# Kernel optimization log

Hardware: AMD Instinct MI355X
Metric: run time of the kernel (lower is better)

Reference implementation:

```python
import jax, jax.numpy as jnp
import numpy as np

D_MODEL = 1024
N_HIDDEN = 64   # per-head dim (outer factor of packed proj dim)
N_HEAD = 16
B, L = 2, 2048


def setup_inputs() -> dict:
    key = jax.random.key(0)
    ks = jax.random.split(key, 7)
    s = 0.02
    return {
        "q": jax.random.normal(ks[0], (B, L, D_MODEL), dtype=jnp.float32),
        "k": jax.random.normal(ks[1], (B, L, D_MODEL), dtype=jnp.float32),
        "v": jax.random.normal(ks[2], (B, L, D_MODEL), dtype=jnp.float32),
        # torch nn.Linear weights: shape (out_features, in_features), y = x @ W.T
        "W_Q": jax.random.normal(ks[3], (N_HIDDEN * N_HEAD, D_MODEL), dtype=jnp.float32) * s,
        "W_K": jax.random.normal(ks[4], (N_HIDDEN * N_HEAD, D_MODEL), dtype=jnp.float32) * s,
        "W_V": jax.random.normal(ks[5], (N_HIDDEN * N_HEAD, D_MODEL), dtype=jnp.float32) * s,
        "W_O": jax.random.normal(ks[6], (D_MODEL, N_HEAD * N_HIDDEN), dtype=jnp.float32) * s,
    }


def reference(q, k, v, W_Q, W_K, W_V, W_O):
    b, l, _ = q.shape
    # projections (bias=False)
    qp = q @ W_Q.T  # [b,l,n_hidden*n_head]
    kp = k @ W_K.T
    vp = v @ W_V.T
    # rearrange 'b l (c h) -> b l c h' with c=n_hidden: hidden is OUTER factor
    qh = qp.reshape(b, l, N_HIDDEN, N_HEAD)
    kh = kp.reshape(b, l, N_HIDDEN, N_HEAD)
    vh = vp.reshape(b, l, N_HIDDEN, N_HEAD)
    scores = jnp.einsum('bldh,bjdh->bhlj', qh, kh) / np.float32(np.sqrt(N_HIDDEN))
    attn = jax.nn.softmax(scores, axis=-1)
    out = jnp.einsum('bhlj,bjdh->bldh', attn, vh)  # [b,l,n_hidden,n_head]
    out = out.reshape(b, l, N_HIDDEN * N_HEAD)      # 'b l d h -> b l (d h)'
    return out @ W_O.T
```

## Files before the change

### kernel.cpp

```cpp
#include <hip/hip_runtime.h>
#include <hip/hip_bf16.h>
#include <stdint.h>

typedef __attribute__((ext_vector_type(8))) short short8;
typedef __attribute__((ext_vector_type(4))) float f32x4;
typedef __attribute__((ext_vector_type(16))) float f32x16;
typedef __attribute__((ext_vector_type(2))) int int2v;
typedef unsigned short u16;
typedef unsigned int u32;


#define WAIT_VM12() do { asm volatile("s_waitcnt vmcnt(12)" ::: "memory"); \
                         __builtin_amdgcn_sched_barrier(0); } while (0)
#define WAIT_VM8()  do { asm volatile("s_waitcnt vmcnt(8)" ::: "memory"); \
                         __builtin_amdgcn_sched_barrier(0); } while (0)
#define WAIT_VM0()  do { asm volatile("s_waitcnt vmcnt(0)" ::: "memory"); \
                         __builtin_amdgcn_sched_barrier(0); } while (0)
#define BARRIER()   do { __builtin_amdgcn_s_barrier(); \
                         __builtin_amdgcn_sched_barrier(0); } while (0)
#define LGKM0_BAR() do { asm volatile("s_waitcnt lgkmcnt(0)" ::: "memory"); \
                         __builtin_amdgcn_s_barrier(); \
                         __builtin_amdgcn_sched_barrier(0); } while (0)

__device__ __forceinline__ u16 bf16rne(float f) {
  u32 u = __builtin_bit_cast(u32, f);
  u += 0x7FFFu + ((u >> 16) & 1u);
  return (u16)(u >> 16);
}

__device__ __forceinline__ u32 cvtpk(float lo, float hi) {
  u32 r;
  asm("v_cvt_pk_bf16_f32 %0, %1, %2" : "=v"(r) : "v"(lo), "v"(hi));
  return r;
}

__device__ __forceinline__ void gl_lds16(const u16* g, u16* l) {
  __builtin_amdgcn_global_load_lds((const __attribute__((address_space(1))) void*)g,
                                   (__attribute__((address_space(3))) void*)l, 16, 0, 0);
}

struct CastArgs {
  const float* src[4];
  u16* dst[4];
  int n4[4];
};

__global__ void cast_all(CastArgs a) {
  const int id = blockIdx.y;
  const float* __restrict__ s = a.src[id];
  u16* __restrict__ d = a.dst[id];
  const int stride = gridDim.x * blockDim.x;
  const int i0 = blockIdx.x * blockDim.x + threadIdx.x;
  if (id < 3) {
    const int n4 = a.n4[id];
    for (int i = i0; i < n4; i += stride) {
      float4 v = ((const float4*)s)[i];
      u32 lo = (u32)bf16rne(v.x) | ((u32)bf16rne(v.y) << 16);
      u32 hi = (u32)bf16rne(v.z) | ((u32)bf16rne(v.w) << 16);
      ((uint2*)d)[i] = make_uint2(lo, hi);
    }
  } else {
    const int n = a.n4[3];
    for (int i = i0; i < n; i += stride) {
      int row = i >> 10, c = i & 1023;
      int hh = c >> 6, dd = c & 63;
      d[i] = bf16rne(s[(row << 10) + dd * 16 + hh]);
    }
  }
}

struct ProjFArgs { const float* A[3]; const u16* W[3]; u16* D[3]; float scale[3]; };

__global__ __launch_bounds__(256, 2) void gemm_projf(ProjFArgs pa) {
  const int bid = blockIdx.x;
  const int grp = ((bid >> 6) << 3) | (bid & 7);
  const int bn = ((bid >> 3) & 7) * 128;
  const int z = grp >> 5;
  const int bm = (grp & 31) * 128;
  const float* __restrict__ A = pa.A[z];
  const u16* __restrict__ Bw = pa.W[z];
  u16* __restrict__ D = pa.D[z];
  const float ascale = pa.scale[z];
  const int epi = (z == 2) ? 1 : 0;

  const int tid = threadIdx.x, lane = tid & 63, w = tid >> 6;
  const int wr = w >> 1, wc = w & 1;
  __shared__ __align__(16) u16 As[2][128 * 64];
  __shared__ __align__(16) u16 Bs[2][128 * 64];

  f32x4 acc[4][4];
#pragma unroll
  for (int m = 0; m < 4; ++m)
#pragma unroll
    for (int n = 0; n < 4; ++n) acc[m][n] = (f32x4){0.f, 0.f, 0.f, 0.f};

  struct ARegs { float4 v[8]; };
  ARegs RA, RB;

  auto STAGE_A = [&](int kt, ARegs& R) {
#pragma unroll
    for (int i = 0; i < 4; ++i) {
      int c = tid + i * 256;
      int row = c >> 3;
      int col = (((c & 7) ^ (row & 7)) << 3);
      const float* src = A + (size_t)(bm + row) * 1024 + kt * 64 + col;
      R.v[2 * i] = *(const float4*)(src);
      R.v[2 * i + 1] = *(const float4*)(src + 4);
    }
  };
  auto WRITE_A = [&](ARegs& R, int b) {
#pragma unroll
    for (int i = 0; i < 4; ++i) {
      int c = tid + i * 256;
      u32 p0 = (u32)bf16rne(R.v[2 * i].x) | ((u32)bf16rne(R.v[2 * i].y) << 16);
      u32 p1 = (u32)bf16rne(R.v[2 * i].z) | ((u32)bf16rne(R.v[2 * i].w) << 16);
      u32 p2 = (u32)bf16rne(R.v[2 * i + 1].x) | ((u32)bf16rne(R.v[2 * i + 1].y) << 16);
      u32 p3 = (u32)bf16rne(R.v[2 * i + 1].z) | ((u32)bf16rne(R.v[2 * i + 1].w) << 16);
      *(uint4*)&As[b][c * 8] = make_uint4(p0, p1, p2, p3);
    }
  };
  auto STAGE_B = [&](int kt, int b) {
#pragma unroll
    for (int i = 0; i < 4; ++i) {
      int c = tid + i * 256;
      int row = c >> 3;
      int swz = (((c & 7) ^ (row & 7)) << 3);
      gl_lds16(Bw + (size_t)(bn + row) * 1024 + kt * 64 + swz, &Bs[b][c * 8]);
    }
  };
  auto COMPUTE = [&](int b) {
#pragma unroll
    for (int ks = 0; ks < 2; ++ks) {
      const int ck = ks * 4 + (lane >> 4);
      short8 af[4], bfr[4];
#pragma unroll
      for (int m = 0; m < 4; ++m) {
        int r = wr * 64 + m * 16 + (lane & 15);
        af[m] = *(const short8*)&As[b][(r * 8 + (ck ^ (r & 7))) * 8];
      }
#pragma unroll
      for (int n = 0; n < 4; ++n) {
        int r = wc * 64 + n * 16 + (lane & 15);
        bfr[n] = *(const short8*)&Bs[b][(r * 8 + (ck ^ (r & 7))) * 8];
      }
#pragma unroll
      for (int m = 0; m < 4; ++m)
#pragma unroll
        for (int n = 0; n < 4; ++n)
          acc[m][n] = __builtin_amdgcn_mfma_f32_16x16x32_bf16(af[m], bfr[n], acc[m][n], 0, 0, 0);
    }
  };

  STAGE_A(0, RA); STAGE_B(0, 0);
  STAGE_A(1, RB); STAGE_B(1, 1);
  for (int k2 = 0; k2 < 7; ++k2) {
    const int kt = 2 * k2;
    WAIT_VM12();
    WRITE_A(RA, 0); LGKM0_BAR();
    COMPUTE(0); BARRIER();
    STAGE_A(kt + 2, RA); STAGE_B(kt + 2, 0);
    WAIT_VM12();
    WRITE_A(RB, 1); LGKM0_BAR();
    COMPUTE(1); BARRIER();
    STAGE_A(kt + 3, RB); STAGE_B(kt + 3, 1);
  }
  WAIT_VM12();
  WRITE_A(RA, 0); LGKM0_BAR();
  COMPUTE(0); BARRIER();
  WAIT_VM0();
  WRITE_A(RB, 1); LGKM0_BAR();
  COMPUTE(1);

  const int lrow4 = (lane >> 4) << 2;
  const int h = lane & 15;
  if (epi == 0) {
    const int dbase = (bn + wc * 64) >> 4;
#pragma unroll
    for (int m = 0; m < 4; ++m)
#pragma unroll
      for (int i = 0; i < 4; ++i) {
        int R = bm + wr * 64 + m * 16 + lrow4 + i;
        int b = R >> 11, l = R & 2047;
        u32 lo = (u32)bf16rne(acc[m][0][i] * ascale) | ((u32)bf16rne(acc[m][1][i] * ascale) << 16);
        u32 hi = (u32)bf16rne(acc[m][2][i] * ascale) | ((u32)bf16rne(acc[m][3][i] * ascale) << 16);
        size_t addr = ((size_t)((b * 16 + h) * 2048 + l)) * 64 + dbase;
        *(uint2*)(D + addr) = make_uint2(lo, hi);
      }
  } else {
    const int dbase = (bn + wc * 64) >> 4;
    const int b = bm >> 11;
#pragma unroll
    for (int m = 0; m < 4; ++m) {
      int l0 = (bm & 2047) + wr * 64 + m * 16 + lrow4;
#pragma unroll
      for (int n = 0; n < 4; ++n) {
        int d = dbase + n;
        u32 lo = (u32)bf16rne(acc[m][n][0]) | ((u32)bf16rne(acc[m][n][1]) << 16);
        u32 hi = (u32)bf16rne(acc[m][n][2]) | ((u32)bf16rne(acc[m][n][3]) << 16);
        size_t addr = ((size_t)((b * 16 + h) * 64 + d)) * 2048 + l0;
        *(uint2*)(D + addr) = make_uint2(lo, hi);
      }
    }
  }
}

__global__ __launch_bounds__(256, 2) void gemm_oproj(const u16* __restrict__ A,
                                                     const u16* __restrict__ Bw,
                                                     float* __restrict__ C) {
  const int bn = blockIdx.x * 128, bm = blockIdx.y * 128;
  const int tid = threadIdx.x, lane = tid & 63, w = tid >> 6;
  const int wr = w >> 1, wc = w & 1;
  __shared__ __align__(16) u16 As[2][128 * 64];
  __shared__ __align__(16) u16 Bs[2][128 * 64];
  f32x4 acc[4][4];
#pragma unroll
  for (int m = 0; m < 4; ++m)
#pragma unroll
    for (int n = 0; n < 4; ++n) acc[m][n] = (f32x4){0.f, 0.f, 0.f, 0.f};

  auto STAGE = [&](int kt, int b) {
#pragma unroll
    for (int i = 0; i < 4; ++i) {
      int c = tid + i * 256;
      int row = c >> 3, kc = c & 7;
      int swz = (kc ^ (row & 7)) << 3;
      int bA = bm >> 11;
      int lrow = (bm & 2047) + row;
      const u16* srcA = A + ((size_t)(bA * 16 + kt) * 2048 + lrow) * 64 + swz;
      gl_lds16(srcA, &As[b][c * 8]);
      const u16* srcB = Bw + (size_t)(bn + row) * 1024 + kt * 64 + swz;
      gl_lds16(srcB, &Bs[b][c * 8]);
    }
  };

  auto COMPUTE = [&](int b) {
#pragma unroll
    for (int ks = 0; ks < 2; ++ks) {
      const int ck = ks * 4 + (lane >> 4);
      short8 af[4], bfr[4];
#pragma unroll
      for (int m = 0; m < 4; ++m) {
        int r = wr * 64 + m * 16 + (lane & 15);
        af[m] = *(const short8*)&As[b][(r * 8 + (ck ^ (r & 7))) * 8];
      }
#pragma unroll
      for (int n = 0; n < 4; ++n) {
        int r = wc * 64 + n * 16 + (lane & 15);
        bfr[n] = *(const short8*)&Bs[b][(r * 8 + (ck ^ (r & 7))) * 8];
      }
#pragma unroll
      for (int m = 0; m < 4; ++m)
#pragma unroll
        for (int n = 0; n < 4; ++n)
          acc[m][n] = __builtin_amdgcn_mfma_f32_16x16x32_bf16(af[m], bfr[n], acc[m][n], 0, 0, 0);
    }
  };

  STAGE(0, 0);
  STAGE(1, 1);
  for (int kt = 0; kt < 15; ++kt) {
    WAIT_VM8();
    BARRIER();
    COMPUTE(kt & 1);
    BARRIER();
    if (kt < 14) STAGE(kt + 2, kt & 1);
  }
  WAIT_VM0();
  BARRIER();
  COMPUTE(1);

  const int lrow4 = (lane >> 4) << 2;
#pragma unroll
  for (int m = 0; m < 4; ++m)
#pragma unroll
    for (int i = 0; i < 4; ++i) {
      int R = bm + wr * 64 + m * 16 + lrow4 + i;
      size_t base = (size_t)R * 1024 + bn + wc * 64 + (lane & 15);
#pragma unroll
      for (int n = 0; n < 4; ++n) C[base + n * 16] = acc[m][n][i];
    }
}

__global__ __launch_bounds__(128, 2) void attn_kernel(const u16* __restrict__ Qh,
                                                      const u16* __restrict__ Kh,
                                                      const u16* __restrict__ Vt,
                                                      u16* __restrict__ Oh) {
  const int hb = blockIdx.x;
  const int qt = blockIdx.y;
  const int tid = threadIdx.x, lane = tid & 63, w = tid >> 6;
  const int l31 = lane & 31, hi = lane >> 5;
  __shared__ __align__(16) u16 Ks[2][64 * 64];
  __shared__ __align__(16) u16 Vs[3][64 * 64];

  const u16* Qg = Qh + (size_t)hb * (2048 * 64);
  const u16* Kg = Kh + (size_t)hb * (2048 * 64);
  const u16* Vg = Vt + (size_t)hb * (64 * 2048);
  const int qrow = qt * 64 + w * 32 + l31;

  short8 qf[4];
#pragma unroll
  for (int ks = 0; ks < 4; ++ks)
    qf[ks] = *(const short8*)(Qg + (size_t)qrow * 64 + ks * 16 + hi * 8);

  int rs[4], sw[4];
#pragma unroll
  for (int i = 0; i < 4; ++i) {
    int c = tid + i * 128;
    rs[i] = c >> 3;
    sw[i] = (((c & 7) ^ (rs[i] & 7)) << 3);
  }

  auto STAGE_K = [&](int t, int slot) {
    const size_t ko = (size_t)t * (64 * 64);
#pragma unroll
    for (int i = 0; i < 4; ++i) {
      int c = tid + i * 128;
      gl_lds16(Kg + ko + (size_t)rs[i] * 64 + sw[i], &Ks[slot][c * 8]);
    }
  };
  auto STAGE_V = [&](int t, int slot) {
    const int vo = t * 64;
#pragma unroll
    for (int i = 0; i < 4; ++i) {
      int c = tid + i * 128;
      gl_lds16(Vg + (size_t)rs[i] * 2048 + vo + sw[i], &Vs[slot][c * 8]);
    }
  };

  f32x16 oacc0, oacc1, SA0, SA1, SB0, SB1;
#pragma unroll
  for (int i = 0; i < 16; ++i) { oacc0[i] = 0.f; oacc1[i] = 0.f; }
  u32 pkA[16], pkB[16];
  float lrow = 0.f;

  auto QKT = [&](int kslot, f32x16& s0, f32x16& s1) {
#pragma unroll
    for (int i = 0; i < 16; ++i) { s0[i] = 0.f; s1[i] = 0.f; }
    __builtin_amdgcn_s_setprio(1);
#pragma unroll
    for (int ks = 0; ks < 4; ++ks) {
      const int ck = 2 * ks + hi;
      const int r0 = l31, r1 = 32 + l31;
      short8 k0 = *(const short8*)&Ks[kslot][(r0 * 8 + (ck ^ (r0 & 7))) * 8];
      short8 k1 = *(const short8*)&Ks[kslot][(r1 * 8 + (ck ^ (r1 & 7))) * 8];
      s0 = __builtin_amdgcn_mfma_f32_32x32x16_bf16(k0, qf[ks], s0, 0, 0, 0);
      s1 = __builtin_amdgcn_mfma_f32_32x32x16_bf16(k1, qf[ks], s1, 0, 0, 0);
    }
    __builtin_amdgcn_s_setprio(0);
  };

  auto PV = [&](const u32* pk, int vslot) {
    __builtin_amdgcn_s_setprio(1);
#pragma unroll
    for (int c = 0; c < 4; ++c) {
      union { u32 wu[4]; short8 v; } un;
      un.wu[0] = pk[c * 4 + 0]; un.wu[1] = pk[c * 4 + 1];
      un.wu[2] = pk[c * 4 + 2]; un.wu[3] = pk[c * 4 + 3];
      const int ckv = 2 * c + hi;
      const int rv0 = l31, rv1 = 32 + l31;
      short8 v0 = *(const short8*)&Vs[vslot][(rv0 * 8 + (ckv ^ (rv0 & 7))) * 8];
      short8 v1 = *(const short8*)&Vs[vslot][(rv1 * 8 + (ckv ^ (rv1 & 7))) * 8];
      oacc0 = __builtin_amdgcn_mfma_f32_32x32x16_bf16(v0, un.v, oacc0, 0, 0, 0);
      oacc1 = __builtin_amdgcn_mfma_f32_32x32x16_bf16(v1, un.v, oacc1, 0, 0, 0);
    }
    __builtin_amdgcn_s_setprio(0);
  };

  auto SOFTMAX = [&](f32x16& s0, f32x16& s1, u32* pk) {
#pragma unroll
    for (int i = 0; i < 16; ++i) {
      s0[i] = __builtin_amdgcn_exp2f(s0[i]);
      s1[i] = __builtin_amdgcn_exp2f(s1[i]);
    }
    f32x16 a01 = s0 + s1;
    float r8[8];
#pragma unroll
    for (int i = 0; i < 8; ++i) r8[i] = a01[i] + a01[i + 8];
#pragma unroll
    for (int i = 0; i < 4; ++i) r8[i] += r8[i + 4];
    float rsum = (r8[0] + r8[1]) + (r8[2] + r8[3]);
    int2v pr = __builtin_amdgcn_permlane32_swap(__builtin_bit_cast(int, rsum),
                                                __builtin_bit_cast(int, rsum), false, false);
    lrow += __builtin_bit_cast(float, pr[0]) + __builtin_bit_cast(float, pr[1]);
#pragma unroll
    for (int c = 0; c < 4; ++c) {
      float pe0, pe1, pe2, pe3, pe4, pe5, pe6, pe7;
      if (c < 2) {
        const int s8 = (c & 1) * 8;
        pe0 = s0[s8 + 0]; pe1 = s0[s8 + 1]; pe2 = s0[s8 + 2]; pe3 = s0[s8 + 3];
        pe4 = s0[s8 + 4]; pe5 = s0[s8 + 5]; pe6 = s0[s8 + 6]; pe7 = s0[s8 + 7];
      } else {
        const int s8 = (c & 1) * 8;
        pe0 = s1[s8 + 0]; pe1 = s1[s8 + 1]; pe2 = s1[s8 + 2]; pe3 = s1[s8 + 3];
        pe4 = s1[s8 + 4]; pe5 = s1[s8 + 5]; pe6 = s1[s8 + 6]; pe7 = s1[s8 + 7];
      }
      u32 a0 = cvtpk(pe0, pe1), a1 = cvtpk(pe2, pe3);
      u32 a2 = cvtpk(pe4, pe5), a3 = cvtpk(pe6, pe7);
      int2v w02 = __builtin_amdgcn_permlane32_swap((int)a0, (int)a2, false, false);
      int2v w13 = __builtin_amdgcn_permlane32_swap((int)a1, (int)a3, false, false);
      pk[c * 4 + 0] = (u32)w02[0]; pk[c * 4 + 1] = (u32)w13[0];
      pk[c * 4 + 2] = (u32)w02[1]; pk[c * 4 + 3] = (u32)w13[1];
    }
  };

  STAGE_K(0, 0); STAGE_K(1, 1); STAGE_V(0, 0);
  WAIT_VM8(); BARRIER();
  QKT(0, SA0, SA1);
  BARRIER();
  STAGE_K(2, 0); STAGE_V(1, 1);
  WAIT_VM8(); BARRIER();
  QKT(1, SB0, SB1);
  SOFTMAX(SA0, SA1, pkB);
  BARRIER();
  STAGE_K(3, 1); STAGE_V(2, 2);

  for (int i = 2; i < 32; i += 2) {
    WAIT_VM8(); BARRIER();
    QKT(0, SA0, SA1);
    PV(pkB, (i - 2) % 3);
    SOFTMAX(SB0, SB1, pkA);
    BARRIER();
    if (i + 2 <= 31) STAGE_K(i + 2, 0);
    STAGE_V(i + 1, (i + 1) % 3);
    WAIT_VM8(); BARRIER();
    QKT(1, SB0, SB1);
    PV(pkA, (i - 1) % 3);
    SOFTMAX(SA0, SA1, pkB);
    BARRIER();
    if (i + 3 <= 31) STAGE_K(i + 3, 1);
    if (i + 2 <= 31) STAGE_V(i + 2, (i + 2) % 3);
  }

  WAIT_VM0(); BARRIER();
  SOFTMAX(SB0, SB1, pkA);
  PV(pkB, 30 % 3);
  PV(pkA, 31 % 3);

  const float inv = 1.0f / lrow;
  u16* Og = Oh + (size_t)hb * (2048 * 64) + (size_t)qrow * 64;
#pragma unroll
  for (int dblk = 0; dblk < 2; ++dblk) {
#pragma unroll
    for (int r = 0; r < 16; r += 2) {
      const int d = dblk * 32 + (r & 3) + 8 * (r >> 2) + 4 * hi;
      float v0 = (dblk ? oacc1[r] : oacc0[r]) * inv;
      float v1 = (dblk ? oacc1[r + 1] : oacc0[r + 1]) * inv;
      *(u32*)(Og + d) = (u32)bf16rne(v0) | ((u32)bf16rne(v1) << 16);
    }
  }
}

extern "C" void kernel_launch(void* const* d_in, const int* in_sizes, int n_in,
                              void* d_out, int out_size, void* d_ws, size_t ws_size,
                              hipStream_t stream) {
  const float* q = (const float*)d_in[0];
  const float* k = (const float*)d_in[1];
  const float* v = (const float*)d_in[2];
  const float* WQ = (const float*)d_in[3];
  const float* WK = (const float*)d_in[4];
  const float* WV = (const float*)d_in[5];
  const float* WO = (const float*)d_in[6];
  float* out = (float*)d_out;
  char* ws = (char*)d_ws;
  const size_t MB = 1024 * 1024;
  if (ws_size < 64 * MB) return;

  u16* WQb = (u16*)(ws + 24 * MB);
  u16* WKb = (u16*)(ws + 26 * MB);
  u16* WVb = (u16*)(ws + 28 * MB);
  u16* WOt = (u16*)(ws + 30 * MB);
  u16* Qh  = (u16*)(ws + 32 * MB);
  u16* Kh  = (u16*)(ws + 40 * MB);
  u16* Vt  = (u16*)(ws + 48 * MB);
  u16* Ohd = (u16*)(ws + 56 * MB);

  CastArgs ca;
  ca.src[0] = WQ; ca.dst[0] = WQb; ca.n4[0] = (1024 * 1024) / 4;
  ca.src[1] = WK; ca.dst[1] = WKb; ca.n4[1] = (1024 * 1024) / 4;
  ca.src[2] = WV; ca.dst[2] = WVb; ca.n4[2] = (1024 * 1024) / 4;
  ca.src[3] = WO; ca.dst[3] = WOt; ca.n4[3] = 1024 * 1024;
  cast_all<<<dim3(128, 4), 256, 0, stream>>>(ca);

  ProjFArgs pa;
  pa.A[0] = q; pa.W[0] = WQb; pa.D[0] = Qh;  pa.scale[0] = 0.18033688011f;
  pa.A[1] = k; pa.W[1] = WKb; pa.D[1] = Kh;  pa.scale[1] = 1.0f;
  pa.A[2] = v; pa.W[2] = WVb; pa.D[2] = Vt;  pa.scale[2] = 1.0f;
  gemm_projf<<<768, 256, 0, stream>>>(pa);

  attn_kernel<<<dim3(32, 32), 128, 0, stream>>>(Qh, Kh, Vt, Ohd);

  gemm_oproj<<<dim3(8, 32), 256, 0, stream>>>(Ohd, WOt, out);
}
```

Before: 131.1 us.

## Split attention KV range across two blocks and merge with atomics

The attention kernel now uses 256-thread blocks covering 128 query rows and splits the key/value sequence into two halves along a new grid dimension. Each block accumulates unnormalized outputs and row sums into fp32 workspace via atomicAdd. A new normalization kernel then divides by the summed row sum and packs the result to bf16. This aims to improve K/V tile reuse and load balance. In exchange it adds memsets of the workspace, many fp32 global atomics, and an extra kernel launch, and the LDS swizzle is adjusted for the new staging pattern.

Result: slower. 332.3 us (+153.4%).

```diff
diff --git a/kernel.cpp b/kernel.cpp
--- a/kernel.cpp
+++ b/kernel.cpp
@@ -13,6 +13,8 @@
 #define WAIT_VM12() do { asm volatile("s_waitcnt vmcnt(12)" ::: "memory"); \
                          __builtin_amdgcn_sched_barrier(0); } while (0)
 #define WAIT_VM8()  do { asm volatile("s_waitcnt vmcnt(8)" ::: "memory"); \
+                         __builtin_amdgcn_sched_barrier(0); } while (0)
+#define WAIT_VM4()  do { asm volatile("s_waitcnt vmcnt(4)" ::: "memory"); \
                          __builtin_amdgcn_sched_barrier(0); } while (0)
 #define WAIT_VM0()  do { asm volatile("s_waitcnt vmcnt(0)" ::: "memory"); \
                          __builtin_amdgcn_sched_barrier(0); } while (0)
@@ -281,48 +283,50 @@
     }
 }
 
-__global__ __launch_bounds__(128, 2) void attn_kernel(const u16* __restrict__ Qh,
+__global__ __launch_bounds__(256, 2) void attn_kernel(const u16* __restrict__ Qh,
                                                       const u16* __restrict__ Kh,
                                                       const u16* __restrict__ Vt,
-                                                      u16* __restrict__ Oh) {
+                                                      float* __restrict__ Of,
+                                                      float* __restrict__ Lp) {
   const int hb = blockIdx.x;
   const int qt = blockIdx.y;
+  const int half = blockIdx.z;
   const int tid = threadIdx.x, lane = tid & 63, w = tid >> 6;
   const int l31 = lane & 31, hi = lane >> 5;
   __shared__ __align__(16) u16 Ks[2][64 * 64];
   __shared__ __align__(16) u16 Vs[3][64 * 64];
 
   const u16* Qg = Qh + (size_t)hb * (2048 * 64);
-  const u16* Kg = Kh + (size_t)hb * (2048 * 64);
-  const u16* Vg = Vt + (size_t)hb * (64 * 2048);
-  const int qrow = qt * 64 + w * 32 + l31;
+  const u16* Kg = Kh + (size_t)hb * (2048 * 64) + (size_t)half * 1024 * 64;
+  const u16* Vg = Vt + (size_t)hb * (64 * 2048) + half * 1024;
+  const int qrow = qt * 128 + w * 32 + l31;
 
   short8 qf[4];
 #pragma unroll
   for (int ks = 0; ks < 4; ++ks)
     qf[ks] = *(const short8*)(Qg + (size_t)qrow * 64 + ks * 16 + hi * 8);
 
-  int rs[4], sw[4];
-#pragma unroll
-  for (int i = 0; i < 4; ++i) {
-    int c = tid + i * 128;
+  int rs[2], sw[2];
+#pragma unroll
+  for (int i = 0; i < 2; ++i) {
+    int c = tid + i * 256;
     rs[i] = c >> 3;
-    sw[i] = (((c & 7) ^ (rs[i] & 7)) << 3);
+    sw[i] = (((c & 7) ^ ((rs[i] ^ (rs[i] >> 3)) & 7)) << 3);
   }
 
   auto STAGE_K = [&](int t, int slot) {
     const size_t ko = (size_t)t * (64 * 64);
 #pragma unroll
-    for (int i = 0; i < 4; ++i) {
-      int c = tid + i * 128;
+    for (int i = 0; i < 2; ++i) {
+      int c = tid + i * 256;
       gl_lds16(Kg + ko + (size_t)rs[i] * 64 + sw[i], &Ks[slot][c * 8]);
     }
   };
   auto STAGE_V = [&](int t, int slot) {
     const int vo = t * 64;
 #pragma unroll
-    for (int i = 0; i < 4; ++i) {
-      int c = tid + i * 128;
+    for (int i = 0; i < 2; ++i) {
+      int c = tid + i * 256;
       gl_lds16(Vg + (size_t)rs[i] * 2048 + vo + sw[i], &Vs[slot][c * 8]);
     }
   };
@@ -341,8 +345,8 @@
     for (int ks = 0; ks < 4; ++ks) {
       const int ck = 2 * ks + hi;
       const int r0 = l31, r1 = 32 + l31;
-      short8 k0 = *(const short8*)&Ks[kslot][(r0 * 8 + (ck ^ (r0 & 7))) * 8];
-      short8 k1 = *(const short8*)&Ks[kslot][(r1 * 8 + (ck ^ (r1 & 7))) * 8];
+      short8 k0 = *(const short8*)&Ks[kslot][(r0 * 8 + (ck ^ ((r0 ^ (r0 >> 3)) & 7))) * 8];
+      short8 k1 = *(const short8*)&Ks[kslot][(r1 * 8 + (ck ^ ((r1 ^ (r1 >> 3)) & 7))) * 8];
       s0 = __builtin_amdgcn_mfma_f32_32x32x16_bf16(k0, qf[ks], s0, 0, 0, 0);
       s1 = __builtin_amdgcn_mfma_f32_32x32x16_bf16(k1, qf[ks], s1, 0, 0, 0);
     }
@@ -358,8 +362,8 @@
       un.wu[2] = pk[c * 4 + 2]; un.wu[3] = pk[c * 4 + 3];
       const int ckv = 2 * c + hi;
       const int rv0 = l31, rv1 = 32 + l31;
-      short8 v0 = *(const short8*)&Vs[vslot][(rv0 * 8 + (ckv ^ (rv0 & 7))) * 8];
-      short8 v1 = *(const short8*)&Vs[vslot][(rv1 * 8 + (ckv ^ (rv1 & 7))) * 8];
+      short8 v0 = *(const short8*)&Vs[vslot][(rv0 * 8 + (ckv ^ ((rv0 ^ (rv0 >> 3)) & 7))) * 8];
+      short8 v1 = *(const short8*)&Vs[vslot][(rv1 * 8 + (ckv ^ ((rv1 ^ (rv1 >> 3)) & 7))) * 8];
       oacc0 = __builtin_amdgcn_mfma_f32_32x32x16_bf16(v0, un.v, oacc0, 0, 0, 0);
       oacc1 = __builtin_amdgcn_mfma_f32_32x32x16_bf16(v1, un.v, oacc1, 0, 0, 0);
     }
@@ -404,50 +408,64 @@
   };
 
   STAGE_K(0, 0); STAGE_K(1, 1); STAGE_V(0, 0);
-  WAIT_VM8(); BARRIER();
+  WAIT_VM4(); BARRIER();
   QKT(0, SA0, SA1);
   BARRIER();
   STAGE_K(2, 0); STAGE_V(1, 1);
-  WAIT_VM8(); BARRIER();
+  WAIT_VM4(); BARRIER();
   QKT(1, SB0, SB1);
   SOFTMAX(SA0, SA1, pkB);
   BARRIER();
   STAGE_K(3, 1); STAGE_V(2, 2);
 
-  for (int i = 2; i < 32; i += 2) {
-    WAIT_VM8(); BARRIER();
+  for (int i = 2; i < 16; i += 2) {
+    WAIT_VM4(); BARRIER();
     QKT(0, SA0, SA1);
     PV(pkB, (i - 2) % 3);
     SOFTMAX(SB0, SB1, pkA);
     BARRIER();
-    if (i + 2 <= 31) STAGE_K(i + 2, 0);
+    if (i + 2 <= 15) STAGE_K(i + 2, 0);
     STAGE_V(i + 1, (i + 1) % 3);
-    WAIT_VM8(); BARRIER();
+    WAIT_VM4(); BARRIER();
     QKT(1, SB0, SB1);
     PV(pkA, (i - 1) % 3);
     SOFTMAX(SA0, SA1, pkB);
     BARRIER();
-    if (i + 3 <= 31) STAGE_K(i + 3, 1);
-    if (i + 2 <= 31) STAGE_V(i + 2, (i + 2) % 3);
+    if (i + 3 <= 15) STAGE_K(i + 3, 1);
+    if (i + 2 <= 15) STAGE_V(i + 2, (i + 2) % 3);
   }
 
   WAIT_VM0(); BARRIER();
   SOFTMAX(SB0, SB1, pkA);
-  PV(pkB, 30 % 3);
-  PV(pkA, 31 % 3);
-
-  const float inv = 1.0f / lrow;
-  u16* Og = Oh + (size_t)hb * (2048 * 64) + (size_t)qrow * 64;
+  PV(pkB, 14 % 3);
+  PV(pkA, 15 % 3);
+
+  float* Ofb = Of + ((size_t)hb * 2048 + qrow) * 64;
 #pragma unroll
   for (int dblk = 0; dblk < 2; ++dblk) {
 #pragma unroll
-    for (int r = 0; r < 16; r += 2) {
+    for (int r = 0; r < 16; ++r) {
       const int d = dblk * 32 + (r & 3) + 8 * (r >> 2) + 4 * hi;
-      float v0 = (dblk ? oacc1[r] : oacc0[r]) * inv;
-      float v1 = (dblk ? oacc1[r + 1] : oacc0[r + 1]) * inv;
-      *(u32*)(Og + d) = (u32)bf16rne(v0) | ((u32)bf16rne(v1) << 16);
-    }
-  }
+      atomicAdd(&Ofb[d], (dblk ? oacc1[r] : oacc0[r]));
+    }
+  }
+  if (hi == 0) atomicAdd(&Lp[hb * 2048 + qrow], lrow);
+}
+
+__global__ void attn_norm(const float* __restrict__ Of, const float* __restrict__ Lp,
+                          u16* __restrict__ Ohd) {
+  const int tid = threadIdx.x;
+  const int row = blockIdx.x * 32 + (tid >> 3);
+  const int o8 = (tid & 7) * 8;
+  const float inv = 1.0f / Lp[row];
+  const float* src = Of + (size_t)row * 64 + o8;
+  float4 a = *(const float4*)src;
+  float4 b = *(const float4*)(src + 4);
+  u32 p0 = (u32)bf16rne(a.x * inv) | ((u32)bf16rne(a.y * inv) << 16);
+  u32 p1 = (u32)bf16rne(a.z * inv) | ((u32)bf16rne(a.w * inv) << 16);
+  u32 p2 = (u32)bf16rne(b.x * inv) | ((u32)bf16rne(b.y * inv) << 16);
+  u32 p3 = (u32)bf16rne(b.z * inv) | ((u32)bf16rne(b.w * inv) << 16);
+  *(uint4*)(Ohd + (size_t)row * 64 + o8) = make_uint4(p0, p1, p2, p3);
 }
 
 extern "C" void kernel_launch(void* const* d_in, const int* in_sizes, int n_in,
@@ -465,6 +483,8 @@
   const size_t MB = 1024 * 1024;
   if (ws_size < 64 * MB) return;
 
+  float* Of = (float*)(ws + 0 * MB);
+  float* Lp = (float*)(ws + 16 * MB);
   u16* WQb = (u16*)(ws + 24 * MB);
   u16* WKb = (u16*)(ws + 26 * MB);
   u16* WVb = (u16*)(ws + 28 * MB);
@@ -474,6 +494,9 @@
   u16* Vt  = (u16*)(ws + 48 * MB);
   u16* Ohd = (u16*)(ws + 56 * MB);
 
+  hipMemsetAsync(Of, 0, 16 * MB, stream);
+  hipMemsetAsync(Lp, 0, 65536 * sizeof(float), stream);
+
   CastArgs ca;
   ca.src[0] = WQ; ca.dst[0] = WQb; ca.n4[0] = (1024 * 1024) / 4;
   ca.src[1] = WK; ca.dst[1] = WKb; ca.n4[1] = (1024 * 1024) / 4;
@@ -487,7 +510,9 @@
   pa.A[2] = v; pa.W[2] = WVb; pa.D[2] = Vt;  pa.scale[2] = 1.0f;
   gemm_projf<<<768, 256, 0, stream>>>(pa);
 
-  attn_kernel<<<dim3(32, 32), 128, 0, stream>>>(Qh, Kh, Vt, Ohd);
+  attn_kernel<<<dim3(32, 16, 2), 256, 0, stream>>>(Qh, Kh, Vt, Of, Lp);
+
+  attn_norm<<<2048, 256, 0, stream>>>(Of, Lp, Ohd);
 
   gemm_oproj<<<dim3(8, 32), 256, 0, stream>>>(Ohd, WOt, out);
 }
```
